# Optimization experiments

Hardware: AMD Instinct MI355X
Metric: run time of the kernel (lower is better)

## Reference

```python
import jax, jax.numpy as jnp
import numpy as np
import math

H = 512      # d_model
N = 64       # d_state
B = 16
L = 4096
DT_MIN, DT_MAX = 0.001, 0.1


def setup_inputs() -> dict:
    key = jax.random.key(0)
    ks = jax.random.split(key, 6)
    u = jax.random.normal(ks[0], (B, H, L), dtype=jnp.float32)
    # S4DKernel parameters
    C = jax.random.normal(ks[1], (H, N // 2, 2), dtype=jnp.float32)  # view_as_real of cfloat C
    log_dt = (jax.random.uniform(ks[2], (H,), dtype=jnp.float32)
              * (math.log(DT_MAX) - math.log(DT_MIN)) + math.log(DT_MIN))
    log_A_real = jnp.log(0.5 * jnp.ones((H, N // 2), dtype=jnp.float32))
    A_imag = math.pi * jnp.broadcast_to(jnp.arange(N // 2, dtype=jnp.float32), (H, N // 2))
    # S4D parameters
    D = jax.random.normal(ks[3], (H,), dtype=jnp.float32)
    # output_linear: Conv1d(H, 2H, kernel_size=1) -> weight (2H, H), bias (2H,)
    W = jax.random.normal(ks[4], (2 * H, H), dtype=jnp.float32) * (1.0 / math.sqrt(H))
    b = jax.random.normal(ks[5], (2 * H,), dtype=jnp.float32) * 0.01
    return {"u": u, "C": C, "log_dt": log_dt, "log_A_real": log_A_real,
            "A_imag": A_imag, "D": D, "W": W, "b": b}


def _s4d_kernel(C, log_dt, log_A_real, A_imag, L):
    """Generate the (H, L) convolution kernel from diagonal SSM parameters."""
    dt = jnp.exp(log_dt)                                    # (H,)
    Cc = C[..., 0] + 1j * C[..., 1]                         # (H, N/2) complex
    A = -jnp.exp(log_A_real) + 1j * A_imag                  # (H, N/2)
    dtA = A * dt[:, None]                                   # (H, N/2)
    # Vandermonde: exp(dtA * l) for l in [0, L)
    K = jnp.exp(dtA[:, :, None] * jnp.arange(L, dtype=jnp.float32))  # (H, N/2, L)
    Cw = Cc * (jnp.exp(dtA) - 1.0) / A                      # (H, N/2)
    k = 2.0 * jnp.einsum('hn,hnl->hl', Cw, K).real          # (H, L)
    return k


def reference(u, C, log_dt, log_A_real, A_imag, D, W, b):
    Lc = u.shape[-1]
    k = _s4d_kernel(C, log_dt, log_A_real, A_imag, Lc)      # (H, L)
    # FFT long convolution (linear conv via zero-padding to 2L)
    k_f = jnp.fft.rfft(k, n=2 * Lc)                          # (H, L+1)
    u_f = jnp.fft.rfft(u, n=2 * Lc)                          # (B, H, L+1)
    y = jnp.fft.irfft(u_f * k_f, n=2 * Lc)[..., :Lc]         # (B, H, L)
    y = y + u * D[:, None]
    y = jax.nn.gelu(y, approximate=False)                    # torch nn.GELU default
    # output_linear: 1x1 Conv1d (H -> 2H) then GLU over channel dim
    z = jnp.einsum('oh,bhl->bol', W, y) + b[None, :, None]   # (B, 2H, L)
    a, g = jnp.split(z, 2, axis=1)
    return a * jax.nn.sigmoid(g)                             # (B, H, L)
```

## Files before the change

kernel.cpp:

```cpp
#include <hip/hip_runtime.h>

#define BB 16
#define HH 512
#define NH 32
#define LL 4096
#define TCH 64
#define NCH 64
#define KA 128

static_assert(TCH * NCH == LL, "chunking");

typedef __attribute__((ext_vector_type(8))) short bf16x8;
typedef __attribute__((ext_vector_type(4))) float f32x4;

static __device__ __forceinline__ unsigned short f2bf(float x) {
    return __builtin_bit_cast(unsigned short, (__bf16)x);
}
static __device__ __forceinline__ float bf2f(unsigned short b) {
    return __builtin_bit_cast(float, ((unsigned)b) << 16);
}
static __device__ __forceinline__ unsigned pack2(float a, float b) {
    return (unsigned)f2bf(a) | ((unsigned)f2bf(b) << 16);
}
static __device__ __forceinline__ float gelu1(float x) {
    float a = fmaf(0.071354816f * x, x * x, 1.5957691f * x);
    return x * __builtin_amdgcn_rcpf(1.0f + __expf(-a));
}
static __device__ __forceinline__ unsigned gelu_pk(unsigned p) {
    float a = gelu1(bf2f((unsigned short)(p & 0xffffu)));
    float b = gelu1(bf2f((unsigned short)(p >> 16)));
    return pack2(a, b);
}

static __device__ __forceinline__ void gload_lds16(const void* g, void* l) {
#if __has_builtin(__builtin_amdgcn_global_load_lds)
    __builtin_amdgcn_global_load_lds(
        (const __attribute__((address_space(1))) unsigned int*)g,
        (__attribute__((address_space(3))) unsigned int*)l, 16, 0, 0);
#else
    *(uint4*)l = *(const uint4*)g;
#endif
}

__global__ void k0_params(const float* __restrict__ C,
                          const float* __restrict__ log_dt,
                          const float* __restrict__ lAr,
                          const float* __restrict__ Aim,
                          float* __restrict__ c2R,  float* __restrict__ c2I,
                          float* __restrict__ ltR,  float* __restrict__ ltI,
                          float* __restrict__ xrA,  float* __restrict__ xiA)
{
    int tid = blockIdx.x * 256 + threadIdx.x;
    if (tid >= HH * NH) return;
    int h = tid >> 5;
    float dt = expf(log_dt[h]);
    float Ar = -expf(lAr[tid]);
    float Ai = Aim[tid];
    float xr = Ar * dt, xi = Ai * dt;
    xrA[tid] = xr; xiA[tid] = xi;
    float er = expf(xr);
    float lr = er * cosf(xi);
    float li = er * sinf(xi);
    float wr = lr - 1.0f, wi = li;
    float inv = 1.0f / (Ar * Ar + Ai * Ai);
    float qr = (wr * Ar + wi * Ai) * inv;
    float qi = (wi * Ar - wr * Ai) * inv;
    float cr = C[2 * tid], ci = C[2 * tid + 1];
    c2R[tid] =  2.0f * (cr * qr - ci * qi);
    c2I[tid] = -2.0f * (cr * qi + ci * qr);
    float eT = expf((float)TCH * xr);
    float aT = (float)TCH * xi;
    ltR[tid] = eT * cosf(aT);
    ltI[tid] = eT * sinf(aT);
}

__global__ void kw_pack(const float* __restrict__ W, const float* __restrict__ bias,
                        unsigned short* __restrict__ Wp, float* __restrict__ bp)
{
    int tid = blockIdx.x * 256 + threadIdx.x;
    int drow = tid >> 6;
    int kc = (tid & 63) * 8;
    int src = (drow & 1) ? (drow >> 1) + HH : (drow >> 1);
    const float4* s = (const float4*)(W + (size_t)src * HH + kc);
    float4 a = s[0], b4 = s[1];
    uint4 pack;
    pack.x = pack2(a.x, a.y);
    pack.y = pack2(a.z, a.w);
    pack.z = pack2(b4.x, b4.y);
    pack.w = pack2(b4.z, b4.w);
    *(uint4*)(Wp + (size_t)drow * HH + kc) = pack;
    if (tid < 2 * HH)
        bp[tid] = bias[(tid & 1) ? (tid >> 1) + HH : (tid >> 1)];
}

__global__ __launch_bounds__(64) void kA_build(
    const float* __restrict__ c2R, const float* __restrict__ c2I,
    const float* __restrict__ xrA, const float* __restrict__ xiA,
    const float* __restrict__ Dv,
    unsigned short* __restrict__ Apan, unsigned short* __restrict__ Vpan)
{
    int h = blockIdx.x;
    int t = threadIdx.x;
    __shared__ float s_xr[NH], s_xi[NH], s_cr[NH], s_ci[NH], s_k[TCH];
    if (t < NH) {
        s_xr[t] = xrA[h * NH + t]; s_xi[t] = xiA[h * NH + t];
        s_cr[t] = c2R[h * NH + t]; s_ci[t] = c2I[h * NH + t];
    }
    __syncthreads();
    {
        float d = (float)t;
        float acc = 0.f;
#pragma unroll
        for (int n = 0; n < NH; ++n) {
            float er = __expf(s_xr[n] * d);
            float sv, cv; __sincosf(s_xi[n] * d, &sv, &cv);
            acc = fmaf(s_cr[n], er * cv, fmaf(s_ci[n], er * sv, acc));
        }
        s_k[t] = acc;
    }
    __syncthreads();
    float k0d = s_k[0] + Dv[h];
    unsigned short row[KA];
#pragma unroll
    for (int tau = 0; tau < TCH; ++tau)
        row[tau] = f2bf((tau < t) ? s_k[t - tau] : (tau == t ? k0d : 0.f));
    float tp = (float)(t + 1);
#pragma unroll
    for (int n = 0; n < NH; ++n) {
        float er = __expf(s_xr[n] * tp);
        float sv, cv; __sincosf(s_xi[n] * tp, &sv, &cv);
        float pr = er * cv, pi = er * sv;
        row[TCH + 2 * n]     = f2bf(fmaf(s_cr[n], pr,  s_ci[n] * pi));
        row[TCH + 2 * n + 1] = f2bf(fmaf(s_ci[n], pr, -s_cr[n] * pi));
    }
    {
        uint4* dst = (uint4*)(Apan + ((size_t)h * TCH + t) * KA);
        const uint4* src = (const uint4*)row;
#pragma unroll
        for (int i = 0; i < 16; ++i) dst[i] = src[i];
    }
    {
        int n = t >> 1, cm = t & 1;
        float xr = s_xr[n], xi = s_xi[n];
        unsigned short vrow[TCH];
#pragma unroll
        for (int tau = 0; tau < TCH; ++tau) {
            float p = (float)(TCH - 1 - tau);
            float er = __expf(xr * p);
            float sv, cv; __sincosf(xi * p, &sv, &cv);
            vrow[tau] = f2bf(cm ? er * sv : er * cv);
        }
        uint4* vd = (uint4*)(Vpan + ((size_t)h * TCH + t) * TCH);
        const uint4* vs = (const uint4*)vrow;
#pragma unroll
        for (int i = 0; i < 8; ++i) vd[i] = vs[i];
    }
}

__global__ __launch_bounds__(256)
__attribute__((amdgpu_waves_per_eu(2)))
void kBCD(
    const float* __restrict__ u,
    const unsigned short* __restrict__ Apan, const unsigned short* __restrict__ Vpan,
    const float* __restrict__ ltR, const float* __restrict__ ltI,
    unsigned short* __restrict__ yb)
{
    __shared__ unsigned short Sl[4][TCH * TCH];
    int h = blockIdx.x & (HH - 1), g = blockIdx.x >> 9;
    int tid = threadIdx.x;
    int lane = tid & 63, w = tid >> 6;
    int b = g * 4 + w;
    int lrow = lane & 15, hi = lane >> 4, lk8 = hi * 8;
    const float* ug = u + ((size_t)b * HH + h) * LL;
    const unsigned short* Ap = Apan + (size_t)h * TCH * KA;
    const unsigned short* Vp = Vpan + (size_t)h * TCH * TCH;
    char* Sw = (char*)Sl[w];

    bf16x8 ub[2][4];
#pragma unroll
    for (int ks = 0; ks < 2; ++ks)
#pragma unroll
        for (int n = 0; n < 4; ++n) {
            int c = n * 16 + lrow;
            const float* up = ug + c * TCH + ks * 32 + lk8;
            float4 f0 = *(const float4*)up, f1 = *(const float4*)(up + 4);
            bf16x8 v;
            v[0]=f2bf(f0.x); v[1]=f2bf(f0.y); v[2]=f2bf(f0.z); v[3]=f2bf(f0.w);
            v[4]=f2bf(f1.x); v[5]=f2bf(f1.y); v[6]=f2bf(f1.z); v[7]=f2bf(f1.w);
            ub[ks][n] = v;
        }

#pragma unroll
    for (int m = 0; m < 4; ++m) {
        f32x4 accE[4];
#pragma unroll
        for (int n = 0; n < 4; ++n) { f32x4 z = {0.f,0.f,0.f,0.f}; accE[n] = z; }
#pragma unroll
        for (int ks = 0; ks < 2; ++ks) {
            bf16x8 vf = *(const bf16x8*)(Vp + (m * 16 + lrow) * TCH + ks * 32 + lk8);
#pragma unroll
            for (int n = 0; n < 4; ++n)
                accE[n] = __builtin_amdgcn_mfma_f32_16x16x32_bf16(vf, ub[ks][n], accE[n], 0, 0, 0);
        }
        int j0 = m * 16 + hi * 4;
#pragma unroll
        for (int n = 0; n < 4; ++n) {
            int c = n * 16 + lrow;
            uint2 p; p.x = pack2(accE[n][0], accE[n][1]); p.y = pack2(accE[n][2], accE[n][3]);
            *(uint2*)(Sw + c * 128 + ((2 * j0) ^ ((c & 7) << 4))) = p;
        }
    }
    asm volatile("s_waitcnt lgkmcnt(0)" ::: "memory");

    if (lane < NH) {
        int n = lane;
        float ar = ltR[h * NH + n], ai = ltI[h * NH + n];
        float sr = 0.f, si = 0.f;
#pragma unroll
        for (int gg = 0; gg < 8; ++gg) {
            unsigned ev[8];
#pragma unroll
            for (int k = 0; k < 8; ++k)
                ev[k] = *(const unsigned*)(Sw + (gg * 8 + k) * 128 + ((4 * n) ^ (k << 4)));
#pragma unroll
            for (int k = 0; k < 8; ++k) {
                *(unsigned*)(Sw + (gg * 8 + k) * 128 + ((4 * n) ^ (k << 4))) = pack2(sr, si);
                float er = bf2f((unsigned short)(ev[k] & 0xffffu));
                float ei = bf2f((unsigned short)(ev[k] >> 16));
                float nsr = fmaf(ar, sr, fmaf(-ai, si, er));
                float nsi = fmaf(ar, si, fmaf(ai, sr, ei));
                sr = nsr; si = nsi;
            }
        }
    }
    asm volatile("s_waitcnt lgkmcnt(0)" ::: "memory");

    bf16x8 sfr[2][4];
#pragma unroll
    for (int ks = 0; ks < 2; ++ks)
#pragma unroll
        for (int n = 0; n < 4; ++n) {
            int c = n * 16 + lrow;
            sfr[ks][n] = *(const bf16x8*)(Sw + c * 128 + ((ks * 64 + lk8 * 2) ^ ((c & 7) << 4)));
        }

    uint2 yp[4][4];
#pragma unroll
    for (int m = 0; m < 4; ++m) {
        f32x4 acc[4];
#pragma unroll
        for (int n = 0; n < 4; ++n) { f32x4 z = {0.f,0.f,0.f,0.f}; acc[n] = z; }
#pragma unroll
        for (int ks = 0; ks < 2; ++ks) {
            bf16x8 af = *(const bf16x8*)(Ap + (m * 16 + lrow) * KA + ks * 32 + lk8);
#pragma unroll
            for (int n = 0; n < 4; ++n)
                acc[n] = __builtin_amdgcn_mfma_f32_16x16x32_bf16(af, ub[ks][n], acc[n], 0, 0, 0);
        }
#pragma unroll
        for (int ks = 0; ks < 2; ++ks) {
            bf16x8 af = *(const bf16x8*)(Ap + (m * 16 + lrow) * KA + 64 + ks * 32 + lk8);
#pragma unroll
            for (int n = 0; n < 4; ++n)
                acc[n] = __builtin_amdgcn_mfma_f32_16x16x32_bf16(af, sfr[ks][n], acc[n], 0, 0, 0);
        }
#pragma unroll
        for (int n = 0; n < 4; ++n) {
            yp[m][n].x = pack2(acc[n][0], acc[n][1]);
            yp[m][n].y = pack2(acc[n][2], acc[n][3]);
        }
    }
    asm volatile("s_waitcnt lgkmcnt(0)" ::: "memory");

#pragma unroll
    for (int m = 0; m < 4; ++m) {
        int t0b = m * 32 + hi * 8;
#pragma unroll
        for (int n = 0; n < 4; ++n) {
            int c = n * 16 + lrow;
            *(uint2*)(Sw + c * 128 + (t0b ^ ((c & 7) << 4))) = yp[m][n];
        }
    }
    asm volatile("s_waitcnt lgkmcnt(0)" ::: "memory");
    unsigned short* yrow = yb + ((size_t)b * HH + h) * LL;
#pragma unroll
    for (int it = 0; it < 8; ++it) {
        int o = it * 1024 + lane * 16;
        int c = o >> 7;
        int sl = o & 127;
        uint4 v = *(const uint4*)(Sw + c * 128 + (sl ^ ((c & 7) << 4)));
        *(uint4*)((char*)yrow + o) = v;
    }
}

__global__ __launch_bounds__(256) void kT_transpose(
    const unsigned short* __restrict__ yb, unsigned short* __restrict__ yt)
{
    __shared__ unsigned short T[64][130];
    int bid = blockIdx.x;
    int lt = bid & 31;
    int ht = (bid >> 5) & 7;
    int b  = bid >> 8;
    int t = threadIdx.x;
#pragma unroll
    for (int r = 0; r < 4; ++r) {
        int chunk = r * 256 + t;
        int row = chunk >> 4;
        int c16 = chunk & 15;
        uint4 v = *(const uint4*)(yb + ((size_t)(b * HH + ht * 64 + row)) * LL
                                     + lt * 128 + c16 * 8);
        v.x = gelu_pk(v.x); v.y = gelu_pk(v.y);
        v.z = gelu_pk(v.z); v.w = gelu_pk(v.w);
        *(uint4*)&T[row][c16 * 8] = v;
    }
    __syncthreads();
    int oct = t & 7, lgrp = t >> 3;
    size_t obase = ((size_t)b * LL + (size_t)lt * 128) * HH + ht * 64 + oct * 8;
#pragma unroll
    for (int r = 0; r < 2; ++r) {
        int l = (r * 32 + lgrp) * 2;
        unsigned v[8];
#pragma unroll
        for (int k = 0; k < 8; ++k)
            v[k] = *(const unsigned*)&T[oct * 8 + k][l];
        uint4 w0, w1;
        w0.x = (v[0] & 0xffffu) | (v[1] << 16);
        w0.y = (v[2] & 0xffffu) | (v[3] << 16);
        w0.z = (v[4] & 0xffffu) | (v[5] << 16);
        w0.w = (v[6] & 0xffffu) | (v[7] << 16);
        w1.x = (v[0] >> 16) | (v[1] & 0xffff0000u);
        w1.y = (v[2] >> 16) | (v[3] & 0xffff0000u);
        w1.z = (v[4] >> 16) | (v[5] & 0xffff0000u);
        w1.w = (v[6] >> 16) | (v[7] & 0xffff0000u);
        *(uint4*)(yt + obase + (size_t)l * HH) = w0;
        *(uint4*)(yt + obase + (size_t)(l + 1) * HH) = w1;
    }
}

#define BM 128
#define BN 128
#define BKK 32

__global__ __launch_bounds__(256, 4) void k4_gemm(
    const unsigned short* __restrict__ Wp, const float* __restrict__ bp,
    const unsigned short* __restrict__ yt, float* __restrict__ out)
{
    __shared__ unsigned short As[BM * BKK];
    __shared__ unsigned short Bs[BN * BKK];
    int tid  = threadIdx.x;
    int bidx = (blockIdx.x & 7) * 512 + (blockIdx.x >> 3);
    int mtile = bidx & 7, ntile = bidx >> 3;
    int mbase = mtile * BM, nbase = ntile * BN;
    int lane = tid & 63;
    int wv = tid >> 6;
    int wr = wv >> 1, wc = wv & 1;
    int lrow = lane & 15;
    int hi = lane >> 4;

    f32x4 acc[4][4];
#pragma unroll
    for (int m = 0; m < 4; ++m)
#pragma unroll
        for (int n = 0; n < 4; ++n) { f32x4 z = {0.f,0.f,0.f,0.f}; acc[m][n] = z; }

    for (int kk = 0; kk < HH; kk += BKK) {
#pragma unroll
        for (int p = 0; p < 2; ++p) {
            int chunk = p * 256 + tid;
            int row = chunk >> 2;
            int c16 = chunk & 3;
            int kc  = (c16 ^ ((row >> 1) & 3)) * 8;
            gload_lds16(Wp + (size_t)(mbase + row) * HH + kk + kc, &As[chunk * 8]);
            gload_lds16(yt + (size_t)(nbase + row) * HH + kk + kc, &Bs[chunk * 8]);
        }
        __syncthreads();
        bf16x8 af[4], bfr[4];
#pragma unroll
        for (int m = 0; m < 4; ++m) {
            int row = wr * 64 + m * 16 + lrow;
            int slot = hi ^ ((row >> 1) & 3);
            af[m] = *(const bf16x8*)&As[row * BKK + slot * 8];
        }
#pragma unroll
        for (int nf = 0; nf < 4; ++nf) {
            int row = wc * 64 + nf * 16 + lrow;
            int slot = hi ^ ((row >> 1) & 3);
            bfr[nf] = *(const bf16x8*)&Bs[row * BKK + slot * 8];
        }
#pragma unroll
        for (int m = 0; m < 4; ++m)
#pragma unroll
            for (int nf = 0; nf < 4; ++nf)
                acc[m][nf] = __builtin_amdgcn_mfma_f32_16x16x32_bf16(af[m], bfr[nf], acc[m][nf], 0, 0, 0);
        __syncthreads();
    }
#pragma unroll
    for (int m = 0; m < 4; ++m) {
        int go = mbase + wr * 64 + m * 16 + (hi * 4);
        float4 bv = *(const float4*)(bp + go);
#pragma unroll
        for (int nf = 0; nf < 4; ++nf) {
            int col  = nbase + wc * 64 + nf * 16 + lrow;
            int bcol = col >> 12;
            int lcol = col & (LL - 1);
            f32x4 v = acc[m][nf];
            float a0 = v[0] + bv.x, g0 = v[1] + bv.y;
            float a1 = v[2] + bv.z, g1 = v[3] + bv.w;
            float o0 = a0 / (1.0f + __expf(-g0));
            float o1 = a1 / (1.0f + __expf(-g1));
            size_t ob = ((size_t)bcol * HH + (size_t)(go >> 1)) * LL + lcol;
            out[ob] = o0;
            out[ob + LL] = o1;
        }
    }
}

extern "C" void kernel_launch(void* const* d_in, const int* in_sizes, int n_in,
                              void* d_out, int out_size, void* d_ws, size_t ws_size,
                              hipStream_t stream) {
    const float* u    = (const float*)d_in[0];
    const float* C    = (const float*)d_in[1];
    const float* ldt  = (const float*)d_in[2];
    const float* lar  = (const float*)d_in[3];
    const float* aim  = (const float*)d_in[4];
    const float* Dv   = (const float*)d_in[5];
    const float* W    = (const float*)d_in[6];
    const float* bias = (const float*)d_in[7];
    float* out = (float*)d_out;

    char* w = (char*)d_ws;
    float* c2R = (float*)w; w += (size_t)HH * NH * 4;
    float* c2I = (float*)w; w += (size_t)HH * NH * 4;
    float* ltR = (float*)w; w += (size_t)HH * NH * 4;
    float* ltI = (float*)w; w += (size_t)HH * NH * 4;
    float* xrA = (float*)w; w += (size_t)HH * NH * 4;
    float* xiA = (float*)w; w += (size_t)HH * NH * 4;
    float* bp  = (float*)w; w += (size_t)2 * HH * 4;
    unsigned short* Wp   = (unsigned short*)w; w += (size_t)2 * HH * HH * 2;
    unsigned short* Apan = (unsigned short*)w; w += (size_t)HH * TCH * KA * 2;
    unsigned short* Vpan = (unsigned short*)w; w += (size_t)HH * TCH * TCH * 2;
    unsigned short* yt   = (unsigned short*)w; w += (size_t)BB * LL * HH * 2;

    unsigned short* yb = (unsigned short*)d_out;

    k0_params   <<<dim3(64),   dim3(256), 0, stream>>>(C, ldt, lar, aim, c2R, c2I, ltR, ltI, xrA, xiA);
    kw_pack     <<<dim3(256),  dim3(256), 0, stream>>>(W, bias, Wp, bp);
    kA_build    <<<dim3(512),  dim3(64),  0, stream>>>(c2R, c2I, xrA, xiA, Dv, Apan, Vpan);
    kBCD        <<<dim3(2048), dim3(256), 0, stream>>>(u, Apan, Vpan, ltR, ltI, yb);
    kT_transpose<<<dim3(4096), dim3(256), 0, stream>>>(yb, yt);
    k4_gemm     <<<dim3(4096), dim3(256), 0, stream>>>(Wp, bp, yt, out);
}
```

Before: 184.0 us.

## Enlarge GEMM tiles to 256x256 with double-buffered LDS pipeline

Rewrites the output-projection GEMM from 128x128 tiles with BK=32 and 4 waves to 256x256 tiles with BK=64, 8 waves, and a double-buffered LDS prefetch. Global-to-LDS loads for stage k+2 are issued while stage k computes, with explicit waitcnt and barriers. The larger tile raises arithmetic intensity and cuts reloads of W and y. In exchange it uses 128 KB of LDS and more accumulator registers per thread, which lowers occupancy.

```diff
diff --git a/kernel.cpp b/kernel.cpp
--- a/kernel.cpp
+++ b/kernel.cpp
@@ -337,66 +337,94 @@
     }
 }
 
-#define BM 128
-#define BN 128
-#define BKK 32
-
-__global__ __launch_bounds__(256, 4) void k4_gemm(
+#define NKT4 8
+
+__global__ __launch_bounds__(512, 2) void k4_gemm(
     const unsigned short* __restrict__ Wp, const float* __restrict__ bp,
     const unsigned short* __restrict__ yt, float* __restrict__ out)
 {
-    __shared__ unsigned short As[BM * BKK];
-    __shared__ unsigned short Bs[BN * BKK];
-    int tid  = threadIdx.x;
-    int bidx = (blockIdx.x & 7) * 512 + (blockIdx.x >> 3);
-    int mtile = bidx & 7, ntile = bidx >> 3;
-    int mbase = mtile * BM, nbase = ntile * BN;
+    __shared__ unsigned short As4[2][256 * 64];
+    __shared__ unsigned short Bs4[2][256 * 64];
+    int tid = threadIdx.x;
+    int bidx = (blockIdx.x & 7) * 128 + (blockIdx.x >> 3);
+    int mtile = bidx & 3, ntile = bidx >> 2;
+    int mbase = mtile * 256, nbase = ntile * 256;
     int lane = tid & 63;
     int wv = tid >> 6;
-    int wr = wv >> 1, wc = wv & 1;
+    int wr = wv >> 2, wc = wv & 3;
     int lrow = lane & 15;
     int hi = lane >> 4;
-
-    f32x4 acc[4][4];
-#pragma unroll
-    for (int m = 0; m < 4; ++m)
+    int rx = (lrow & 7) << 4;
+
+#define STAGE4(kt, buf) do {                                                   \
+    _Pragma("unroll")                                                          \
+    for (int rr = 0; rr < 4; ++rr) {                                           \
+        int _r = rr * 64 + (tid >> 3);                                         \
+        int _u = (tid & 7) ^ (_r & 7);                                         \
+        gload_lds16(Wp + (size_t)(mbase + _r) * HH + (kt) * 64 + _u * 8,       \
+                    &As4[buf][_r * 64 + (tid & 7) * 8]);                       \
+        gload_lds16(yt + (size_t)(nbase + _r) * HH + (kt) * 64 + _u * 8,       \
+                    &Bs4[buf][_r * 64 + (tid & 7) * 8]);                       \
+    }                                                                          \
+} while (0)
+
+    f32x4 acc[8][4];
+#pragma unroll
+    for (int m = 0; m < 8; ++m)
 #pragma unroll
         for (int n = 0; n < 4; ++n) { f32x4 z = {0.f,0.f,0.f,0.f}; acc[m][n] = z; }
 
-    for (int kk = 0; kk < HH; kk += BKK) {
-#pragma unroll
-        for (int p = 0; p < 2; ++p) {
-            int chunk = p * 256 + tid;
-            int row = chunk >> 2;
-            int c16 = chunk & 3;
-            int kc  = (c16 ^ ((row >> 1) & 3)) * 8;
-            gload_lds16(Wp + (size_t)(mbase + row) * HH + kk + kc, &As[chunk * 8]);
-            gload_lds16(yt + (size_t)(nbase + row) * HH + kk + kc, &Bs[chunk * 8]);
-        }
-        __syncthreads();
-        bf16x8 af[4], bfr[4];
-#pragma unroll
-        for (int m = 0; m < 4; ++m) {
-            int row = wr * 64 + m * 16 + lrow;
-            int slot = hi ^ ((row >> 1) & 3);
-            af[m] = *(const bf16x8*)&As[row * BKK + slot * 8];
-        }
-#pragma unroll
-        for (int nf = 0; nf < 4; ++nf) {
-            int row = wc * 64 + nf * 16 + lrow;
-            int slot = hi ^ ((row >> 1) & 3);
-            bfr[nf] = *(const bf16x8*)&Bs[row * BKK + slot * 8];
-        }
-#pragma unroll
-        for (int m = 0; m < 4; ++m)
-#pragma unroll
-            for (int nf = 0; nf < 4; ++nf)
-                acc[m][nf] = __builtin_amdgcn_mfma_f32_16x16x32_bf16(af[m], bfr[nf], acc[m][nf], 0, 0, 0);
-        __syncthreads();
-    }
-#pragma unroll
-    for (int m = 0; m < 4; ++m) {
-        int go = mbase + wr * 64 + m * 16 + (hi * 4);
+    STAGE4(0, 0);
+    STAGE4(1, 1);
+    asm volatile("s_waitcnt vmcnt(8)" ::: "memory");
+    asm volatile("s_barrier" ::: "memory");
+
+#pragma unroll 1
+    for (int kt = 0; kt < NKT4; ++kt) {
+        int cur = kt & 1;
+        const char* Ab = (const char*)&As4[cur][0];
+        const char* Bb = (const char*)&Bs4[cur][0];
+        bf16x8 bfr[4][2];
+#pragma unroll
+        for (int n = 0; n < 4; ++n) {
+            int R = wc * 64 + n * 16 + lrow;
+#pragma unroll
+            for (int ks = 0; ks < 2; ++ks)
+                bfr[n][ks] = *(const bf16x8*)(Bb + R * 128 + ((ks * 64 + hi * 16) ^ rx));
+        }
+#pragma unroll
+        for (int q = 0; q < 4; ++q) {
+            bf16x8 af[2][2];
+#pragma unroll
+            for (int mi = 0; mi < 2; ++mi) {
+                int R = wr * 128 + (q * 2 + mi) * 16 + lrow;
+#pragma unroll
+                for (int ks = 0; ks < 2; ++ks)
+                    af[mi][ks] = *(const bf16x8*)(Ab + R * 128 + ((ks * 64 + hi * 16) ^ rx));
+            }
+#pragma unroll
+            for (int mi = 0; mi < 2; ++mi)
+#pragma unroll
+                for (int n = 0; n < 4; ++n)
+#pragma unroll
+                    for (int ks = 0; ks < 2; ++ks)
+                        acc[q * 2 + mi][n] = __builtin_amdgcn_mfma_f32_16x16x32_bf16(
+                            af[mi][ks], bfr[n][ks], acc[q * 2 + mi][n], 0, 0, 0);
+        }
+        asm volatile("s_barrier" ::: "memory");
+        if (kt + 2 < NKT4) {
+            STAGE4(kt + 2, cur);
+            asm volatile("s_waitcnt vmcnt(8)" ::: "memory");
+        } else {
+            asm volatile("s_waitcnt vmcnt(0)" ::: "memory");
+        }
+        asm volatile("s_barrier" ::: "memory");
+    }
+#undef STAGE4
+
+#pragma unroll
+    for (int m = 0; m < 8; ++m) {
+        int go = mbase + wr * 128 + m * 16 + hi * 4;
         float4 bv = *(const float4*)(bp + go);
 #pragma unroll
         for (int nf = 0; nf < 4; ++nf) {
@@ -448,5 +476,5 @@
     kA_build    <<<dim3(512),  dim3(64),  0, stream>>>(c2R, c2I, xrA, xiA, Dv, Apan, Vpan);
     kBCD        <<<dim3(2048), dim3(256), 0, stream>>>(u, Apan, Vpan, ltR, ltI, yb);
     kT_transpose<<<dim3(4096), dim3(256), 0, stream>>>(yb, yt);
-    k4_gemm     <<<dim3(4096), dim3(256), 0, stream>>>(Wp, bp, yt, out);
-}
+    k4_gemm     <<<dim3(1024), dim3(512), 0, stream>>>(Wp, bp, yt, out);
+}
```

Result: faster. 178.2 us (-3.2%).
